# Optimization experiments

Hardware: AMD Instinct MI355X
Metric: run time of the kernel (lower is better)

The kernel has to match this reference:

```python
import jax, jax.numpy as jnp
import numpy as np
import math

EPS = 1e-5  # BatchNorm eps; eval mode with running_mean=0, running_var=1


def maxpool(x, k, p):
    return jax.lax.reduce_window(x, -jnp.inf, jax.lax.max,
                                 (1, 1, k, k), (1, 1, 1, 1),
                                 ((0, 0), (0, 0), (p, p), (p, p)))


def conv1x1(x, w, b=None):
    # x: [B,Cin,H,W], w: [Cout,Cin]
    y = jnp.einsum('oi,bihw->bohw', w, x)
    if b is not None:
        y = y + b[None, :, None, None]
    return y


def bn_eval(x, g, b):
    scale = g / jnp.sqrt(1.0 + EPS)
    return x * scale[None, :, None, None] + b[None, :, None, None]


def setup_inputs() -> dict:
    B, C, H, W = 2, 64, 80, 80
    c1, c2, c3 = 21, 21, 22
    ch = 32  # C//2
    ks = jax.random.split(jax.random.key(0), 16)
    s = 0.05
    inp = {
        'x': jax.random.normal(ks[0], (B, C, H, W), jnp.float32),
        'q1_w': jax.random.normal(ks[1], (c1, c1), jnp.float32) * s,
        'q1_g': jnp.ones((c1,), jnp.float32),
        'q1_b': jnp.zeros((c1,), jnp.float32),
        'q2_w': jax.random.normal(ks[2], (c2, c2), jnp.float32) * s,
        'q2_g': jnp.ones((c2,), jnp.float32),
        'q2_b': jnp.zeros((c2,), jnp.float32),
        'q3_w': jax.random.normal(ks[3], (c3, c3), jnp.float32) * s,
        'q3_g': jnp.ones((c3,), jnp.float32),
        'q3_b': jnp.zeros((c3,), jnp.float32),
        'k_hf_w': jax.random.normal(ks[4], (ch, C), jnp.float32) * s,
        'k_hf_b': jnp.zeros((ch,), jnp.float32),
        'k_lf_w': jax.random.normal(ks[5], (C - ch, C), jnp.float32) * s,
        'k_lf_b': jnp.zeros((C - ch,), jnp.float32),
        'k_fuse_w': jax.random.normal(ks[6], (C, C), jnp.float32) * s,
        'k_fuse_b': jnp.zeros((C,), jnp.float32),
        'v_bn_g': jnp.ones((C,), jnp.float32),
        'v_bn_b': jnp.zeros((C,), jnp.float32),
        'v_w': jax.random.normal(ks[7], (C, C), jnp.float32) * s,
        'v_b': jnp.zeros((C,), jnp.float32),
        'out_w': jax.random.normal(ks[8], (C, C), jnp.float32) * s,
        'out_b': jnp.zeros((C,), jnp.float32),
    }
    return inp


def reference(x, q1_w, q1_g, q1_b, q2_w, q2_g, q2_b, q3_w, q3_g, q3_b,
              k_hf_w, k_hf_b, k_lf_w, k_lf_b, k_fuse_w, k_fuse_b,
              v_bn_g, v_bn_b, v_w, v_b, out_w, out_b):
    B, C, H, W = x.shape
    N = H * W
    c1 = q1_w.shape[0]
    c2 = q2_w.shape[0]
    # Q: ThreeGroupConvQ (split -> 1x1 conv (no bias) -> BN -> ReLU -> concat)
    x1, x2, x3 = jnp.split(x, [c1, c1 + c2], axis=1)
    y1 = jax.nn.relu(bn_eval(conv1x1(x1, q1_w), q1_g, q1_b))
    y2 = jax.nn.relu(bn_eval(conv1x1(x2, q2_w), q2_g, q2_b))
    y3 = jax.nn.relu(bn_eval(conv1x1(x3, q3_w), q3_g, q3_b))
    Q = jnp.concatenate([y1, y2, y3], axis=1)
    # K: ThermalStructureExtractor
    p3 = maxpool(x, 3, 1)
    p5 = maxpool(x, 5, 2)
    low = (p3 + p5) * 0.5
    high = conv1x1(x - low, k_hf_w, k_hf_b)
    lowp = conv1x1(low, k_lf_w, k_lf_b)
    K = conv1x1(jnp.concatenate([high, lowp], axis=1), k_fuse_w, k_fuse_b)
    # V: BN -> 1x1 conv
    V = conv1x1(bn_eval(x, v_bn_g, v_bn_b), v_w, v_b)
    # attention over N = H*W spatial tokens, channel features
    Qc = Q.reshape(B, C, N)
    Kc = K.reshape(B, C, N)
    Vc = V.reshape(B, C, N)
    attn = jax.nn.softmax(
        jnp.einsum('bcn,bcm->bnm', Qc, Kc) / math.sqrt(C), axis=-1)  # [B,N,N]
    out = jnp.einsum('bnm,bcm->bcn', attn, Vc).reshape(B, C, H, W)
    return conv1x1(out, out_w, out_b) + x
```

## Files before the change

### kernel.cpp

```cpp
#include <hip/hip_runtime.h>
#include <hip/hip_bf16.h>


#define BATCH 2
#define CH 64
#define HH 80
#define WW 80
#define NN 6400
#define NT 100
#define KS 5
#define KTPS (NT/KS)
#define EPSV 1e-5f
#define NEGBIG (-1e30f)
#define QP 72
#define LOG2E8 0.18033688f
#define VSP 65

typedef __hip_bfloat16 bf16;
typedef __attribute__((ext_vector_type(8))) short short8;
typedef __attribute__((ext_vector_type(4))) float f4;
#define MFMA16 __builtin_amdgcn_mfma_f32_16x16x32_bf16

__device__ __forceinline__ float b2f(bf16 v){ return __bfloat162float(v); }
__device__ __forceinline__ bf16 f2b(float v){ return __float2bfloat16(v); }
__device__ __forceinline__ float fexp2(float x){
#if __has_builtin(__builtin_amdgcn_exp2f)
  return __builtin_amdgcn_exp2f(x);
#else
  return exp2f(x);
#endif
}

#define OFF_BIAS 0
#define OFF_WH_B 768
#define OFF_LOW_B (768 + 32768)
#define OFF_Q_B   (OFF_LOW_B + BATCH*CH*NN*2)
#define OFF_K_B   (OFF_Q_B   + BATCH*CH*NN*2)
#define OFF_V_B   (OFF_K_B   + BATCH*CH*NN*2)
#define OFF_P_B   (OFF_V_B   + BATCH*CH*NN*2)
#define OFF_ML_B  (OFF_P_B   + BATCH*NT*KS*4096*4)

__global__ __launch_bounds__(256) void setup_fold(
    const float* __restrict__ q1w, const float* __restrict__ q1g, const float* __restrict__ q1b,
    const float* __restrict__ q2w, const float* __restrict__ q2g, const float* __restrict__ q2b,
    const float* __restrict__ q3w, const float* __restrict__ q3g, const float* __restrict__ q3b,
    const float* __restrict__ khw, const float* __restrict__ khb,
    const float* __restrict__ klw, const float* __restrict__ klb,
    const float* __restrict__ kfw, const float* __restrict__ kfb,
    const float* __restrict__ vg,  const float* __restrict__ vbnb,
    const float* __restrict__ vw,  const float* __restrict__ vb,
    float* __restrict__ biasf, bf16* __restrict__ wh)
{
  __shared__ __align__(16) float skf[4096];
  __shared__ __align__(16) float skh[2048];
  __shared__ __align__(16) float skl[2048];

  int tid = threadIdx.x;
  int blk = blockIdx.x;
  #pragma unroll
  for (int i = 0; i < 4; ++i)
    *(float4*)&skf[(i*256 + tid)*4] = *(const float4*)&kfw[(i*256 + tid)*4];
  #pragma unroll
  for (int i = 0; i < 2; ++i) {
    *(float4*)&skh[(i*256 + tid)*4] = *(const float4*)&khw[(i*256 + tid)*4];
    *(float4*)&skl[(i*256 + tid)*4] = *(const float4*)&klw[(i*256 + tid)*4];
  }
  __syncthreads();

  float rs = rsqrtf(1.0f + EPSV);
  bf16* wq   = wh;
  bf16* wvh  = wh + 4096;
  bf16* wa1  = wh + 8192;
  bf16* wa2m = wh + 12288;

  int t = blk*256 + tid;
  int ci = t & 63, co = t >> 6;
  int o = ci*64 + co;

  float w = 0.f, g;
  if (co < 21)      { g = q1g[co];    w = (ci < 21)              ? q1w[co*21 + ci]            : 0.f; }
  else if (co < 42) { g = q2g[co-21]; w = (ci >= 21 && ci < 42)  ? q2w[(co-21)*21 + (ci-21)]  : 0.f; }
  else              { g = q3g[co-42]; w = (ci >= 42)             ? q3w[(co-42)*22 + (ci-42)]  : 0.f; }
  wq[o] = f2b(w * g * rs * LOG2E8);

  float a1 = 0.f, a2 = 0.f;
  #pragma unroll
  for (int j = 0; j < 32; ++j) {
    a1 += skf[co*64 + j]      * skh[j*64 + ci];
    a2 += skf[co*64 + 32 + j] * skl[j*64 + ci];
  }
  wa1[o]  = f2b(a1);
  wa2m[o] = f2b(a2 - a1);
  wvh[o]  = f2b(vw[co*64 + ci] * vg[ci] * rs);

  if (blk == 0 && tid < 64) {
    int c2 = tid;
    float bq;
    if (c2 < 21)      bq = q1b[c2];
    else if (c2 < 42) bq = q2b[c2-21];
    else              bq = q3b[c2-42];
    biasf[c2] = bq * LOG2E8;
    float bk = kfb[c2];
    #pragma unroll
    for (int j = 0; j < 32; ++j) {
      bk += skf[c2*64 + j]      * khb[j];
      bk += skf[c2*64 + 32 + j] * klb[j];
    }
    biasf[64 + c2] = bk;
    float bv = vb[c2];
    for (int ci2 = 0; ci2 < 64; ++ci2) bv += vw[c2*64 + ci2] * vbnb[ci2];
    biasf[128 + c2] = bv;
  }
}

__global__ __launch_bounds__(256) void pool_low(const float* __restrict__ x,
                                                bf16* __restrict__ lowg)
{
  int t4 = (blockIdx.x*256 + threadIdx.x)*4;
  int bc = t4 / NN; int n = t4 % NN;
  int h = n / WW, w0 = n % WW;
  const float* p = x + bc*NN;
  float m5[4], m3[4];
  #pragma unroll
  for (int j=0;j<4;++j){ m5[j]=NEGBIG; m3[j]=NEGBIG; }
  #pragma unroll
  for (int dh = -2; dh <= 2; ++dh) {
    int hh = h + dh; if (hh < 0 || hh >= HH) continue;
    float r[12];
    const float* row = p + hh*WW;
    if (w0 >= 4)      { float4 a = *(const float4*)&row[w0-4]; r[0]=a.x;r[1]=a.y;r[2]=a.z;r[3]=a.w; }
    else              { r[0]=NEGBIG;r[1]=NEGBIG;r[2]=NEGBIG;r[3]=NEGBIG; }
    { float4 a = *(const float4*)&row[w0]; r[4]=a.x;r[5]=a.y;r[6]=a.z;r[7]=a.w; }
    if (w0 + 7 < WW)  { float4 a = *(const float4*)&row[w0+4]; r[8]=a.x;r[9]=a.y;r[10]=a.z;r[11]=a.w; }
    else              { r[8]=NEGBIG;r[9]=NEGBIG;r[10]=NEGBIG;r[11]=NEGBIG; }
    bool in3 = (dh >= -1 && dh <= 1);
    #pragma unroll
    for (int j=0;j<4;++j) {
      float v3 = fmaxf(fmaxf(r[3+j], r[4+j]), r[5+j]);
      float v5 = fmaxf(fmaxf(r[2+j], v3), r[6+j]);
      m5[j] = fmaxf(m5[j], v5);
      if (in3) m3[j] = fmaxf(m3[j], v3);
    }
  }
  ushort4 o;
  o.x = ((__hip_bfloat16_raw)f2b(0.5f*(m3[0]+m5[0]))).x;
  o.y = ((__hip_bfloat16_raw)f2b(0.5f*(m3[1]+m5[1]))).x;
  o.z = ((__hip_bfloat16_raw)f2b(0.5f*(m3[2]+m5[2]))).x;
  o.w = ((__hip_bfloat16_raw)f2b(0.5f*(m3[3]+m5[3]))).x;
  *(ushort4*)&lowg[t4] = o;
}

__global__ __launch_bounds__(256) void qkv_kernel(
    const float* __restrict__ x, const float* __restrict__ biasf,
    const bf16* __restrict__ wh, const bf16* __restrict__ lowg,
    bf16* __restrict__ qgT, bf16* __restrict__ kgT, bf16* __restrict__ vgc)
{
  __shared__ __align__(16) float xs[64*32];
  __shared__ __align__(16) float lows[64*32];
  __shared__ __align__(16) bf16  wbuf[16384];
  __shared__ ushort vs[64*VSP];
  __shared__ float bias[192];

  int tid = threadIdx.x;
  int blk = blockIdx.x;
  int b = blk / (NT*2);
  int rem = blk % (NT*2);
  int tile = rem >> 1, half = rem & 1;
  int n0 = tile*64 + half*32;

  #pragma unroll
  for (int i = 0; i < 8; ++i) {
    int e = i*256 + tid; int c = e >> 5, p = e & 31;
    xs[c*32 + p]   = x[(b*CH + c)*NN + n0 + p];
    lows[c*32 + p] = b2f(lowg[(b*CH + c)*NN + n0 + p]);
  }
  #pragma unroll
  for (int i = 0; i < 16; ++i)
    ((uint2*)wbuf)[i*256 + tid] = ((const uint2*)wh)[i*256 + tid];
  if (tid < 192) bias[tid] = biasf[tid];
  __syncthreads();

  int co = tid & 63, pg = tid >> 6;
  const bf16* wq   = wbuf;
  const bf16* wvh  = wbuf + 4096;
  const bf16* wa1  = wbuf + 8192;
  const bf16* wa2m = wbuf + 12288;

  {
    float bq = bias[co];
    float4 a0 = make_float4(bq,bq,bq,bq), a1v = a0;
    for (int ci = 0; ci < 64; ++ci) {
      float wv = b2f(wq[ci*64 + co]);
      float4 x0 = *(const float4*)&xs[ci*32 + pg*8];
      float4 x1 = *(const float4*)&xs[ci*32 + pg*8 + 4];
      a0.x += wv*x0.x; a0.y += wv*x0.y; a0.z += wv*x0.z; a0.w += wv*x0.w;
      a1v.x += wv*x1.x; a1v.y += wv*x1.y; a1v.z += wv*x1.z; a1v.w += wv*x1.w;
    }
    float q8[8] = {a0.x,a0.y,a0.z,a0.w,a1v.x,a1v.y,a1v.z,a1v.w};
    #pragma unroll
    for (int j=0;j<8;++j)
      qgT[(size_t)(b*NN + n0 + pg*8 + j)*64 + co] = f2b(fmaxf(q8[j], 0.f));
  }
  {
    float bv = bias[128 + co];
    float4 a0 = make_float4(bv,bv,bv,bv), a1v = a0;
    for (int ci = 0; ci < 64; ++ci) {
      float wv = b2f(wvh[ci*64 + co]);
      float4 x0 = *(const float4*)&xs[ci*32 + pg*8];
      float4 x1 = *(const float4*)&xs[ci*32 + pg*8 + 4];
      a0.x += wv*x0.x; a0.y += wv*x0.y; a0.z += wv*x0.z; a0.w += wv*x0.w;
      a1v.x += wv*x1.x; a1v.y += wv*x1.y; a1v.z += wv*x1.z; a1v.w += wv*x1.w;
    }
    float v8[8] = {a0.x,a0.y,a0.z,a0.w,a1v.x,a1v.y,a1v.z,a1v.w};
    #pragma unroll
    for (int j=0;j<8;++j)
      vs[co*VSP + pg*8 + j] = ((__hip_bfloat16_raw)f2b(v8[j])).x;
  }
  __syncthreads();
  {
    int c = tid >> 2, cb = (tid & 3)*8;
    ushort4 o0;
    ushort u[8];
    #pragma unroll
    for (int j=0;j<8;++j) u[j] = vs[c*VSP + cb + j];
    uint4 pk;
    pk.x = (uint)u[0] | ((uint)u[1] << 16);
    pk.y = (uint)u[2] | ((uint)u[3] << 16);
    pk.z = (uint)u[4] | ((uint)u[5] << 16);
    pk.w = (uint)u[6] | ((uint)u[7] << 16);
    *(uint4*)&vgc[(size_t)(b*CH + c)*NN + n0 + cb] = pk;
    (void)o0;
  }
  {
    float bk = bias[64 + co];
    float4 a0 = make_float4(bk,bk,bk,bk), a1v = a0;
    for (int ci = 0; ci < 64; ++ci) {
      float w1 = b2f(wa1[ci*64 + co]);
      float w2 = b2f(wa2m[ci*64 + co]);
      float4 x0 = *(const float4*)&xs[ci*32 + pg*8];
      float4 x1 = *(const float4*)&xs[ci*32 + pg*8 + 4];
      float4 l0 = *(const float4*)&lows[ci*32 + pg*8];
      float4 l1 = *(const float4*)&lows[ci*32 + pg*8 + 4];
      a0.x += w1*x0.x + w2*l0.x; a0.y += w1*x0.y + w2*l0.y;
      a0.z += w1*x0.z + w2*l0.z; a0.w += w1*x0.w + w2*l0.w;
      a1v.x += w1*x1.x + w2*l1.x; a1v.y += w1*x1.y + w2*l1.y;
      a1v.z += w1*x1.z + w2*l1.z; a1v.w += w1*x1.w + w2*l1.w;
    }
    float k8[8] = {a0.x,a0.y,a0.z,a0.w,a1v.x,a1v.y,a1v.z,a1v.w};
    #pragma unroll
    for (int j=0;j<8;++j)
      kgT[(size_t)(b*NN + n0 + pg*8 + j)*64 + co] = f2b(k8[j]);
  }
}

__global__ __launch_bounds__(256) void attn_partial(
    const bf16* __restrict__ qgT, const bf16* __restrict__ kgT, const bf16* __restrict__ vgc,
    float* __restrict__ part, float* __restrict__ pml)
{
  __shared__ __align__(16) char smem[27648];
  bf16* Qld = (bf16*)smem;
  bf16* Pld = (bf16*)smem;
  bf16* Kld = (bf16*)(smem + 9216);
  bf16* Vld = (bf16*)(smem + 18432);

  int tid = threadIdx.x;
  int blk = blockIdx.x;
  int b = blk / (NT*KS);
  int rem = blk % (NT*KS);
  int tile = rem / KS, split = rem % KS;
  int n0 = tile*64;
  int wv = tid >> 6, lane = tid & 63, ln = lane & 15, quad = lane >> 4;
  int arow = (wv*16 + ln)*QP;

  #pragma unroll
  for (int i = 0; i < 4; ++i) {
    int f = (i*256 + tid)*4; int n = f >> 6, c = f & 63;
    *(uint2*)&Qld[n*QP + c] = *(const uint2*)&qgT[(size_t)(b*NN + n0 + n)*64 + c];
  }
  __syncthreads();
  short8 aq0 = *(const short8*)&Qld[arow + quad*8];
  short8 aq1 = *(const short8*)&Qld[arow + 32 + quad*8];

  f4 accO[4];
  float lacc[4];
  #pragma unroll
  for (int t=0;t<4;++t) accO[t] = (f4){0.f,0.f,0.f,0.f};
  #pragma unroll
  for (int r=0;r<4;++r) lacc[r] = 0.f;

  uint2 kreg[4], vreg[4];
  int mbase = split*KTPS*64;
  #pragma unroll
  for (int i = 0; i < 4; ++i) {
    int f = (i*256 + tid)*4; int rr = f >> 6, cc = f & 63;
    kreg[i] = *(const uint2*)&kgT[(size_t)(b*NN + mbase + rr)*64 + cc];
    vreg[i] = *(const uint2*)&vgc[(size_t)(b*CH + rr)*NN + mbase + cc];
  }

  for (int kt = 0; kt < KTPS; ++kt) {
    __syncthreads();
    #pragma unroll
    for (int i = 0; i < 4; ++i) {
      int f = (i*256 + tid)*4; int rr = f >> 6, cc = f & 63;
      *(uint2*)&Kld[rr*QP + cc] = kreg[i];
      *(uint2*)&Vld[rr*QP + cc] = vreg[i];
    }
    __syncthreads();
    if (kt + 1 < KTPS) {
      int m0 = mbase + (kt+1)*64;
      #pragma unroll
      for (int i = 0; i < 4; ++i) {
        int f = (i*256 + tid)*4; int rr = f >> 6, cc = f & 63;
        kreg[i] = *(const uint2*)&kgT[(size_t)(b*NN + m0 + rr)*64 + cc];
        vreg[i] = *(const uint2*)&vgc[(size_t)(b*CH + rr)*NN + m0 + cc];
      }
    }

    f4 accS[4];
    #pragma unroll
    for (int t = 0; t < 4; ++t) {
      short8 bk0 = *(const short8*)&Kld[(t*16+ln)*QP + quad*8];
      short8 bk1 = *(const short8*)&Kld[(t*16+ln)*QP + 32 + quad*8];
      f4 z = (f4){0.f,0.f,0.f,0.f};
      z = MFMA16(aq0, bk0, z, 0, 0, 0);
      accS[t] = MFMA16(aq1, bk1, z, 0, 0, 0);
    }

    #pragma unroll
    for (int r=0;r<4;++r) {
      int n = wv*16 + quad*4 + r;
      #pragma unroll
      for (int t=0;t<4;++t) {
        float p = fexp2(accS[t][r]);
        Pld[n*QP + t*16 + ln] = f2b(p);
        lacc[r] += p;
      }
    }

    short8 ap0 = *(const short8*)&Pld[arow + quad*8];
    short8 ap1 = *(const short8*)&Pld[arow + 32 + quad*8];
    #pragma unroll
    for (int t = 0; t < 4; ++t) {
      short8 bv0 = *(const short8*)&Vld[(t*16+ln)*QP + quad*8];
      short8 bv1 = *(const short8*)&Vld[(t*16+ln)*QP + 32 + quad*8];
      accO[t] = MFMA16(ap0, bv0, accO[t], 0, 0, 0);
      accO[t] = MFMA16(ap1, bv1, accO[t], 0, 0, 0);
    }
  }

  size_t pbase = ((size_t)(b*NT + tile)*KS + split)*4096;
  #pragma unroll
  for (int r=0;r<4;++r) {
    int n = wv*16 + quad*4 + r;
    #pragma unroll
    for (int t=0;t<4;++t)
      part[pbase + n*64 + t*16 + ln] = accO[t][r];
  }
  size_t mlb = ((size_t)(b*NT + tile)*KS + split)*64;
  #pragma unroll
  for (int r=0;r<4;++r) {
    float s = lacc[r];
    s += __shfl_xor(s, 1, 16);
    s += __shfl_xor(s, 2, 16);
    s += __shfl_xor(s, 4, 16);
    s += __shfl_xor(s, 8, 16);
    if (ln == 0) pml[mlb + wv*16 + quad*4 + r] = s;
  }
}

__global__ __launch_bounds__(256) void attn_reduce(
    const float* __restrict__ part, const float* __restrict__ pml,
    const float* __restrict__ x, const float* __restrict__ outw,
    const float* __restrict__ outb, float* __restrict__ out)
{
  __shared__ __align__(16) float Os[32*65];
  __shared__ __align__(16) float Wot[64*65];
  __shared__ float linv[32];

  int tid = threadIdx.x;
  int blk = blockIdx.x;
  int b = blk / (NT*2);
  int rem = blk % (NT*2);
  int tile = rem >> 1, half = rem & 1;
  int nb = half*32;
  size_t base = (size_t)(b*NT + tile)*KS;

  for (int i = 0; i < 16; ++i) {
    int e = i*256 + tid; int co2 = e >> 6, c = e & 63;
    Wot[c*65 + co2] = outw[co2*64 + c];
  }
  if (tid < 32) {
    float l = 0.f;
    #pragma unroll
    for (int s=0;s<KS;++s) l += pml[(base+s)*64 + nb + tid];
    linv[tid] = 1.0f / l;
  }
  __syncthreads();

  #pragma unroll
  for (int i = 0; i < 8; ++i) {
    int e = i*256 + tid; int n = e >> 6, c = e & 63;
    float a = 0.f;
    #pragma unroll
    for (int s=0;s<KS;++s)
      a += part[(base+s)*4096 + (size_t)(nb+n)*64 + c];
    Os[n*65 + c] = a * linv[n];
  }
  __syncthreads();

  {
    int n = tid & 31, cog = tid >> 5;
    float acc[8];
    #pragma unroll
    for (int k=0;k<8;++k) acc[k] = outb[cog*8 + k];
    for (int c = 0; c < 64; ++c) {
      float ov = Os[n*65 + c];
      #pragma unroll
      for (int k=0;k<8;++k) acc[k] += Wot[c*65 + cog*8 + k] * ov;
    }
    #pragma unroll
    for (int k=0;k<8;++k) {
      int co2 = cog*8 + k;
      int idx = (b*CH + co2)*NN + tile*64 + nb + n;
      out[idx] = acc[k] + x[idx];
    }
  }
}

extern "C" void kernel_launch(void* const* d_in, const int* in_sizes, int n_in,
                              void* d_out, int out_size, void* d_ws, size_t ws_size,
                              hipStream_t stream) {
  const float* x    = (const float*)d_in[0];
  const float* q1w  = (const float*)d_in[1];
  const float* q1g  = (const float*)d_in[2];
  const float* q1b  = (const float*)d_in[3];
  const float* q2w  = (const float*)d_in[4];
  const float* q2g  = (const float*)d_in[5];
  const float* q2b  = (const float*)d_in[6];
  const float* q3w  = (const float*)d_in[7];
  const float* q3g  = (const float*)d_in[8];
  const float* q3b  = (const float*)d_in[9];
  const float* khw  = (const float*)d_in[10];
  const float* khb  = (const float*)d_in[11];
  const float* klw  = (const float*)d_in[12];
  const float* klb  = (const float*)d_in[13];
  const float* kfw  = (const float*)d_in[14];
  const float* kfb  = (const float*)d_in[15];
  const float* vbg  = (const float*)d_in[16];
  const float* vbb  = (const float*)d_in[17];
  const float* vw   = (const float*)d_in[18];
  const float* vb   = (const float*)d_in[19];
  const float* outw = (const float*)d_in[20];
  const float* outb = (const float*)d_in[21];

  char*  wsb  = (char*)d_ws;
  float* biasf= (float*)(wsb + OFF_BIAS);
  bf16*  wh   = (bf16*)(wsb + OFF_WH_B);
  bf16*  lowg = (bf16*)(wsb + OFF_LOW_B);
  bf16*  qgT  = (bf16*)(wsb + OFF_Q_B);
  bf16*  kgT  = (bf16*)(wsb + OFF_K_B);
  bf16*  vgc  = (bf16*)(wsb + OFF_V_B);
  float* part = (float*)(wsb + OFF_P_B);
  float* pml  = (float*)(wsb + OFF_ML_B);

  hipLaunchKernelGGL(setup_fold, dim3(16), dim3(256), 0, stream,
                     q1w,q1g,q1b,q2w,q2g,q2b,q3w,q3g,q3b,
                     khw,khb,klw,klb,kfw,kfb,vbg,vbb,vw,vb, biasf, wh);
  hipLaunchKernelGGL(pool_low, dim3(BATCH*CH*NN/1024), dim3(256), 0, stream, x, lowg);
  hipLaunchKernelGGL(qkv_kernel, dim3(BATCH*NT*2), dim3(256), 0, stream,
                     x, biasf, wh, lowg, qgT, kgT, vgc);
  hipLaunchKernelGGL(attn_partial, dim3(BATCH*NT*KS), dim3(256), 0, stream,
                     qgT, kgT, vgc, part, pml);
  hipLaunchKernelGGL(attn_reduce, dim3(BATCH*NT*2), dim3(256), 0, stream,
                     part, pml, x, outw, outb, (float*)d_out);
}
```

Before: 177.3 us.

## Compute transposed S tile, store bf16 partial outputs, reduce row sums via LDS

Swaps the operand roles in the QK^T MFMA so each lane's S accumulators cover consecutive keys. The exp'd probabilities can then be packed and written to LDS as 8-byte vectors instead of scalar bf16 stores. The per-split partial output tiles are written in bf16 instead of fp32, and the reduce kernel reads them as packed vectors, halving partial-buffer traffic. Row sums are now reduced across quads with shuffles and an LDS stage, at the cost of an extra barrier per tile, added bf16 rounding of partial sums, and a transposed partial layout.

New measurement: 173.4 us. -2.2%, faster.

```diff
diff --git a/kernel.cpp b/kernel.cpp
--- a/kernel.cpp
+++ b/kernel.cpp
@@ -23,6 +23,10 @@
 
 __device__ __forceinline__ float b2f(bf16 v){ return __bfloat162float(v); }
 __device__ __forceinline__ bf16 f2b(float v){ return __float2bfloat16(v); }
+__device__ __forceinline__ ushort f2bu(float v){ return ((__hip_bfloat16_raw)__float2bfloat16(v)).x; }
+__device__ __forceinline__ float bu2f(ushort u){
+  union { unsigned int i; float f; } w; w.i = ((unsigned int)u) << 16; return w.f;
+}
 __device__ __forceinline__ float fexp2(float x){
 #if __has_builtin(__builtin_amdgcn_exp2f)
   return __builtin_amdgcn_exp2f(x);
@@ -38,7 +42,7 @@
 #define OFF_K_B   (OFF_Q_B   + BATCH*CH*NN*2)
 #define OFF_V_B   (OFF_K_B   + BATCH*CH*NN*2)
 #define OFF_P_B   (OFF_V_B   + BATCH*CH*NN*2)
-#define OFF_ML_B  (OFF_P_B   + BATCH*NT*KS*4096*4)
+#define OFF_ML_B  (OFF_P_B   + BATCH*NT*KS*4096*2)
 
 __global__ __launch_bounds__(256) void setup_fold(
     const float* __restrict__ q1w, const float* __restrict__ q1g, const float* __restrict__ q1b,
@@ -143,10 +147,10 @@
     }
   }
   ushort4 o;
-  o.x = ((__hip_bfloat16_raw)f2b(0.5f*(m3[0]+m5[0]))).x;
-  o.y = ((__hip_bfloat16_raw)f2b(0.5f*(m3[1]+m5[1]))).x;
-  o.z = ((__hip_bfloat16_raw)f2b(0.5f*(m3[2]+m5[2]))).x;
-  o.w = ((__hip_bfloat16_raw)f2b(0.5f*(m3[3]+m5[3]))).x;
+  o.x = f2bu(0.5f*(m3[0]+m5[0]));
+  o.y = f2bu(0.5f*(m3[1]+m5[1]));
+  o.z = f2bu(0.5f*(m3[2]+m5[2]));
+  o.w = f2bu(0.5f*(m3[3]+m5[3]));
   *(ushort4*)&lowg[t4] = o;
 }
 
@@ -214,12 +218,11 @@
     float v8[8] = {a0.x,a0.y,a0.z,a0.w,a1v.x,a1v.y,a1v.z,a1v.w};
     #pragma unroll
     for (int j=0;j<8;++j)
-      vs[co*VSP + pg*8 + j] = ((__hip_bfloat16_raw)f2b(v8[j])).x;
+      vs[co*VSP + pg*8 + j] = f2bu(v8[j]);
   }
   __syncthreads();
   {
     int c = tid >> 2, cb = (tid & 3)*8;
-    ushort4 o0;
     ushort u[8];
     #pragma unroll
     for (int j=0;j<8;++j) u[j] = vs[c*VSP + cb + j];
@@ -229,7 +232,6 @@
     pk.z = (uint)u[4] | ((uint)u[5] << 16);
     pk.w = (uint)u[6] | ((uint)u[7] << 16);
     *(uint4*)&vgc[(size_t)(b*CH + c)*NN + n0 + cb] = pk;
-    (void)o0;
   }
   {
     float bk = bias[64 + co];
@@ -255,9 +257,10 @@
 
 __global__ __launch_bounds__(256) void attn_partial(
     const bf16* __restrict__ qgT, const bf16* __restrict__ kgT, const bf16* __restrict__ vgc,
-    float* __restrict__ part, float* __restrict__ pml)
+    ushort* __restrict__ part, float* __restrict__ pml)
 {
   __shared__ __align__(16) char smem[27648];
+  __shared__ float lred[256];
   bf16* Qld = (bf16*)smem;
   bf16* Pld = (bf16*)smem;
   bf16* Kld = (bf16*)(smem + 9216);
@@ -278,15 +281,19 @@
     *(uint2*)&Qld[n*QP + c] = *(const uint2*)&qgT[(size_t)(b*NN + n0 + n)*64 + c];
   }
   __syncthreads();
-  short8 aq0 = *(const short8*)&Qld[arow + quad*8];
-  short8 aq1 = *(const short8*)&Qld[arow + 32 + quad*8];
+  short8 bq[4][2];
+  #pragma unroll
+  for (int nt = 0; nt < 4; ++nt) {
+    bq[nt][0] = *(const short8*)&Qld[(nt*16 + ln)*QP + quad*8];
+    bq[nt][1] = *(const short8*)&Qld[(nt*16 + ln)*QP + 32 + quad*8];
+  }
 
   f4 accO[4];
   float lacc[4];
   #pragma unroll
   for (int t=0;t<4;++t) accO[t] = (f4){0.f,0.f,0.f,0.f};
   #pragma unroll
-  for (int r=0;r<4;++r) lacc[r] = 0.f;
+  for (int nt=0;nt<4;++nt) lacc[nt] = 0.f;
 
   uint2 kreg[4], vreg[4];
   int mbase = split*KTPS*64;
@@ -316,26 +323,26 @@
       }
     }
 
+    short8 ak0 = *(const short8*)&Kld[arow + quad*8];
+    short8 ak1 = *(const short8*)&Kld[arow + 32 + quad*8];
     f4 accS[4];
     #pragma unroll
-    for (int t = 0; t < 4; ++t) {
-      short8 bk0 = *(const short8*)&Kld[(t*16+ln)*QP + quad*8];
-      short8 bk1 = *(const short8*)&Kld[(t*16+ln)*QP + 32 + quad*8];
+    for (int nt = 0; nt < 4; ++nt) {
       f4 z = (f4){0.f,0.f,0.f,0.f};
-      z = MFMA16(aq0, bk0, z, 0, 0, 0);
-      accS[t] = MFMA16(aq1, bk1, z, 0, 0, 0);
-    }
-
-    #pragma unroll
-    for (int r=0;r<4;++r) {
-      int n = wv*16 + quad*4 + r;
-      #pragma unroll
-      for (int t=0;t<4;++t) {
-        float p = fexp2(accS[t][r]);
-        Pld[n*QP + t*16 + ln] = f2b(p);
-        lacc[r] += p;
-      }
-    }
+      z = MFMA16(ak0, bq[nt][0], z, 0, 0, 0);
+      accS[nt] = MFMA16(ak1, bq[nt][1], z, 0, 0, 0);
+    }
+    #pragma unroll
+    for (int nt = 0; nt < 4; ++nt) {
+      float p0 = fexp2(accS[nt][0]), p1 = fexp2(accS[nt][1]);
+      float p2 = fexp2(accS[nt][2]), p3 = fexp2(accS[nt][3]);
+      lacc[nt] += (p0 + p1) + (p2 + p3);
+      uint2 pk;
+      pk.x = (uint)f2bu(p0) | ((uint)f2bu(p1) << 16);
+      pk.y = (uint)f2bu(p2) | ((uint)f2bu(p3) << 16);
+      *(uint2*)&Pld[(nt*16 + ln)*QP + wv*16 + quad*4] = pk;
+    }
+    __syncthreads();
 
     short8 ap0 = *(const short8*)&Pld[arow + quad*8];
     short8 ap1 = *(const short8*)&Pld[arow + 32 + quad*8];
@@ -349,27 +356,30 @@
   }
 
   size_t pbase = ((size_t)(b*NT + tile)*KS + split)*4096;
-  #pragma unroll
-  for (int r=0;r<4;++r) {
-    int n = wv*16 + quad*4 + r;
-    #pragma unroll
-    for (int t=0;t<4;++t)
-      part[pbase + n*64 + t*16 + ln] = accO[t][r];
-  }
-  size_t mlb = ((size_t)(b*NT + tile)*KS + split)*64;
-  #pragma unroll
-  for (int r=0;r<4;++r) {
-    float s = lacc[r];
-    s += __shfl_xor(s, 1, 16);
-    s += __shfl_xor(s, 2, 16);
-    s += __shfl_xor(s, 4, 16);
-    s += __shfl_xor(s, 8, 16);
-    if (ln == 0) pml[mlb + wv*16 + quad*4 + r] = s;
+  ushort* pp = part + pbase;
+  #pragma unroll
+  for (int t = 0; t < 4; ++t) {
+    uint2 pk;
+    pk.x = (uint)f2bu(accO[t][0]) | ((uint)f2bu(accO[t][1]) << 16);
+    pk.y = (uint)f2bu(accO[t][2]) | ((uint)f2bu(accO[t][3]) << 16);
+    *(uint2*)&pp[(t*16 + ln)*64 + wv*16 + quad*4] = pk;
+  }
+  #pragma unroll
+  for (int nt = 0; nt < 4; ++nt) {
+    float s = lacc[nt];
+    s += __shfl_xor(s, 16);
+    s += __shfl_xor(s, 32);
+    if (quad == 0) lred[wv*64 + nt*16 + ln] = s;
+  }
+  __syncthreads();
+  if (tid < 64) {
+    size_t mlb = ((size_t)(b*NT + tile)*KS + split)*64;
+    pml[mlb + tid] = (lred[tid] + lred[64 + tid]) + (lred[128 + tid] + lred[192 + tid]);
   }
 }
 
 __global__ __launch_bounds__(256) void attn_reduce(
-    const float* __restrict__ part, const float* __restrict__ pml,
+    const ushort* __restrict__ part, const float* __restrict__ pml,
     const float* __restrict__ x, const float* __restrict__ outw,
     const float* __restrict__ outb, float* __restrict__ out)
 {
@@ -398,13 +408,21 @@
   __syncthreads();
 
   #pragma unroll
-  for (int i = 0; i < 8; ++i) {
-    int e = i*256 + tid; int n = e >> 6, c = e & 63;
-    float a = 0.f;
-    #pragma unroll
-    for (int s=0;s<KS;++s)
-      a += part[(base+s)*4096 + (size_t)(nb+n)*64 + c];
-    Os[n*65 + c] = a * linv[n];
+  for (int j = 0; j < 2; ++j) {
+    int idx = j*256 + tid;
+    int c = idx >> 3, q = idx & 7;
+    float a0=0.f, a1=0.f, a2=0.f, a3=0.f;
+    #pragma unroll
+    for (int s = 0; s < KS; ++s) {
+      uint2 v = *(const uint2*)&part[(base+s)*4096 + (size_t)c*64 + nb + q*4];
+      a0 += bu2f((ushort)(v.x & 0xffff)); a1 += bu2f((ushort)(v.x >> 16));
+      a2 += bu2f((ushort)(v.y & 0xffff)); a3 += bu2f((ushort)(v.y >> 16));
+    }
+    int nl = q*4;
+    Os[(nl+0)*65 + c] = a0 * linv[nl+0];
+    Os[(nl+1)*65 + c] = a1 * linv[nl+1];
+    Os[(nl+2)*65 + c] = a2 * linv[nl+2];
+    Os[(nl+3)*65 + c] = a3 * linv[nl+3];
   }
   __syncthreads();
 
@@ -453,15 +471,15 @@
   const float* outw = (const float*)d_in[20];
   const float* outb = (const float*)d_in[21];
 
-  char*  wsb  = (char*)d_ws;
-  float* biasf= (float*)(wsb + OFF_BIAS);
-  bf16*  wh   = (bf16*)(wsb + OFF_WH_B);
-  bf16*  lowg = (bf16*)(wsb + OFF_LOW_B);
-  bf16*  qgT  = (bf16*)(wsb + OFF_Q_B);
-  bf16*  kgT  = (bf16*)(wsb + OFF_K_B);
-  bf16*  vgc  = (bf16*)(wsb + OFF_V_B);
-  float* part = (float*)(wsb + OFF_P_B);
-  float* pml  = (float*)(wsb + OFF_ML_B);
+  char*   wsb  = (char*)d_ws;
+  float*  biasf= (float*)(wsb + OFF_BIAS);
+  bf16*   wh   = (bf16*)(wsb + OFF_WH_B);
+  bf16*   lowg = (bf16*)(wsb + OFF_LOW_B);
+  bf16*   qgT  = (bf16*)(wsb + OFF_Q_B);
+  bf16*   kgT  = (bf16*)(wsb + OFF_K_B);
+  bf16*   vgc  = (bf16*)(wsb + OFF_V_B);
+  ushort* part = (ushort*)(wsb + OFF_P_B);
+  float*  pml  = (float*)(wsb + OFF_ML_B);
 
   hipLaunchKernelGGL(setup_fold, dim3(16), dim3(256), 0, stream,
                      q1w,q1g,q1b,q2w,q2g,q2b,q3w,q3g,q3b,
```
